# Optimization experiments

Measured on AMD Instinct MI355X. Metric: run time of the kernel, lower is better.

## Reference

```python
import jax, jax.numpy as jnp
import numpy as np

N = 100000
E = 1600000
IN_C = 256
OUT_C = 128


def setup_inputs() -> dict:
    key = jax.random.key(0)
    ks = jax.random.split(key, 8)
    x = jax.random.normal(ks[0], (N, IN_C), dtype=jnp.float32)
    edge_index = jax.random.randint(ks[1], (2, E), 0, N, dtype=jnp.int64)
    # GCNConv params (weight + bias)
    W = jax.random.normal(ks[2], (IN_C, OUT_C), dtype=jnp.float32) / np.sqrt(IN_C)
    b = jnp.zeros((OUT_C,), dtype=jnp.float32)
    # residual Linear params
    Wr = jax.random.normal(ks[3], (IN_C, OUT_C), dtype=jnp.float32) / np.sqrt(IN_C)
    br = jnp.zeros((OUT_C,), dtype=jnp.float32)
    # LayerNorm params
    gamma = jnp.ones((OUT_C,), dtype=jnp.float32)
    beta = jnp.zeros((OUT_C,), dtype=jnp.float32)
    return {"x": x, "edge_index": edge_index, "W": W, "b": b,
            "Wr": Wr, "br": br, "gamma": gamma, "beta": beta}


def _gcn_conv(x, src, dst, W, b):
    # PyG GCNConv: add self-loops, symmetric degree normalization,
    # transform first (out < in), then gather-scale-scatter.
    n = x.shape[0]
    loops = jnp.arange(n, dtype=src.dtype)
    src = jnp.concatenate([src, loops])
    dst = jnp.concatenate([dst, loops])
    ones = jnp.ones_like(dst, dtype=x.dtype)
    deg = jax.ops.segment_sum(ones, dst, num_segments=n)  # [N]
    dinv = jnp.where(deg > 0, jax.lax.rsqrt(deg), 0.0)
    norm = dinv[src] * dinv[dst]                           # [E+N]
    h = x @ W                                              # [N, out]
    msg = h[src] * norm[:, None]                           # [E+N, out]
    agg = jax.ops.segment_sum(msg, dst, num_segments=n)    # [N, out]
    return agg + b


def _layer_norm(x, gamma, beta, eps=1e-5):
    mu = jnp.mean(x, axis=-1, keepdims=True)
    var = jnp.mean(jnp.square(x - mu), axis=-1, keepdims=True)
    return (x - mu) * jax.lax.rsqrt(var + eps) * gamma + beta


def reference(x, edge_index, W, b, Wr, br, gamma, beta):
    src, dst = edge_index[0], edge_index[1]
    res = x @ Wr + br
    h = _gcn_conv(x, src, dst, W, b)
    out = _layer_norm(h + res, gamma, beta)
    return jax.nn.relu(out)
```

## Files before the change

### kernel.cpp

```cpp
#include <hip/hip_runtime.h>

typedef __attribute__((ext_vector_type(8))) short bf16x8;
typedef __attribute__((ext_vector_type(4))) float f32x4;
typedef __attribute__((ext_vector_type(8))) unsigned short ushort8;
typedef __attribute__((ext_vector_type(4))) unsigned short ushort4v;

__device__ __forceinline__ unsigned short f2bf(float f) {
  unsigned int u = __float_as_uint(f);
  u = u + 0x7FFFu + ((u >> 16) & 1u);
  return (unsigned short)(u >> 16);
}
__device__ __forceinline__ float bflo(unsigned int u) { return __uint_as_float(u << 16); }
__device__ __forceinline__ float bfhi(unsigned int u) { return __uint_as_float(u & 0xFFFF0000u); }

#define GLOAD_LDS16(g, l)                                                            \
  __builtin_amdgcn_global_load_lds((const __attribute__((address_space(1))) void*)(g), \
                                   (__attribute__((address_space(3))) void*)(l), 16, 0, 0)

__global__ void k_degrank(const int* __restrict__ dst, int* __restrict__ deg,
                          int* __restrict__ rank, int E) {
  int base = (blockIdx.x * blockDim.x + threadIdx.x) * 4;
  if (base + 3 < E) {
    int4 d = *(const int4*)(dst + base);
    int r0 = atomicAdd(&deg[d.x], 1);
    int r1 = atomicAdd(&deg[d.y], 1);
    int r2 = atomicAdd(&deg[d.z], 1);
    int r3 = atomicAdd(&deg[d.w], 1);
    *(int4*)(rank + base) = make_int4(r0, r1, r2, r3);
  } else {
    for (int e = base; e < E; ++e) rank[e] = atomicAdd(&deg[dst[e]], 1);
  }
}

__global__ void k_dinv(const int* __restrict__ deg, float* __restrict__ dinv, int N) {
  int i = blockIdx.x * blockDim.x + threadIdx.x;
  if (i < N) dinv[i] = rsqrtf((float)(deg[i] + 1));
}

__global__ void k_scanA(const int* __restrict__ deg, int* __restrict__ bsums, int N) {
  __shared__ int s[256];
  int t = threadIdx.x;
  int base = blockIdx.x * 1024 + t * 4;
  int ts = 0;
#pragma unroll
  for (int j = 0; j < 4; ++j) { int idx = base + j; ts += (idx < N) ? deg[idx] : 0; }
  s[t] = ts; __syncthreads();
  for (int off = 1; off < 256; off <<= 1) {
    int v = (t >= off) ? s[t - off] : 0;
    __syncthreads();
    s[t] += v;
    __syncthreads();
  }
  if (t == 255) bsums[blockIdx.x] = s[255];
}

__global__ void k_scanB(int* bsums, int nb) {
  __shared__ int s[128];
  int t = threadIdx.x;
  int v = (t < nb) ? bsums[t] : 0;
  s[t] = v; __syncthreads();
  for (int off = 1; off < 128; off <<= 1) {
    int a = (t >= off) ? s[t - off] : 0;
    __syncthreads();
    s[t] += a;
    __syncthreads();
  }
  if (t < nb) bsums[t] = s[t] - v;
}

__global__ void k_scanC(const int* __restrict__ deg, const int* __restrict__ bsums,
                        int* __restrict__ start, int N) {
  __shared__ int s[256];
  int t = threadIdx.x;
  int base = blockIdx.x * 1024 + t * 4;
  int v[4]; int ts = 0;
#pragma unroll
  for (int j = 0; j < 4; ++j) { int idx = base + j; v[j] = (idx < N) ? deg[idx] : 0; ts += v[j]; }
  s[t] = ts; __syncthreads();
  for (int off = 1; off < 256; off <<= 1) {
    int a = (t >= off) ? s[t - off] : 0;
    __syncthreads();
    s[t] += a;
    __syncthreads();
  }
  int run = bsums[blockIdx.x] + s[t] - ts;
#pragma unroll
  for (int j = 0; j < 4; ++j) { int idx = base + j; if (idx < N) start[idx] = run; run += v[j]; }
}

__global__ void k_fill(const int* __restrict__ src, const int* __restrict__ dst,
                       const int* __restrict__ start, const int* __restrict__ rank,
                       int* __restrict__ ssrc, int E) {
  int base = (blockIdx.x * blockDim.x + threadIdx.x) * 4;
  if (base + 3 < E) {
    int4 d = *(const int4*)(dst + base);
    int4 r = *(const int4*)(rank + base);
    int4 s = *(const int4*)(src + base);
    ssrc[start[d.x] + r.x] = s.x;
    ssrc[start[d.y] + r.y] = s.y;
    ssrc[start[d.z] + r.z] = s.z;
    ssrc[start[d.w] + r.w] = s.w;
  } else {
    for (int e = base; e < E; ++e) ssrc[start[dst[e]] + rank[e]] = src[e];
  }
}

__global__ void k_prepw(const float* __restrict__ W, const float* __restrict__ Wr,
                        unsigned short* __restrict__ Wb) {
  int t = blockIdx.x * 256 + threadIdx.x;
  if (t >= 2048) return;
  int col = t >> 3, g = t & 7;
  const float* Ws = (col < 128) ? (W + col) : (Wr + (col - 128));
#pragma unroll
  for (int kt = 0; kt < 4; ++kt) {
    ushort8 u;
#pragma unroll
    for (int j = 0; j < 8; ++j) u[j] = f2bf(Ws[(size_t)(kt * 64 + g * 8 + j) * 128]);
    *(ushort8*)&Wb[kt * 16384 + col * 64 + ((g ^ (col & 7)) * 8)] = u;
  }
}

__global__ __launch_bounds__(512) void k_gemm(
    const float* __restrict__ x, const unsigned short* __restrict__ Wb,
    const float* __restrict__ br, const float* __restrict__ dinv,
    unsigned short* __restrict__ hs, float* res, int N)
{
  __shared__ unsigned short xt[128][72];
  __shared__ unsigned short wt[256 * 64];
  int tid = threadIdx.x;
  int lane = tid & 63, w = tid >> 6;
  int lo = lane & 15, hi = lane >> 4;
  int brow = blockIdx.x * 128;

  f32x4 acc[16];
#pragma unroll
  for (int c = 0; c < 16; ++c) acc[c] = (f32x4){0.f, 0.f, 0.f, 0.f};

  for (int kt = 0; kt < 4; ++kt) {
    int k0 = kt * 64;
    const unsigned short* gw = Wb + kt * 16384;
#pragma unroll
    for (int i = 0; i < 4; ++i) {
      int off = i * 4096 + tid * 8;
      GLOAD_LDS16(gw + off, &wt[off]);
    }
#pragma unroll
    for (int r = 0; r < 4; ++r) {
      int idx = tid + 512 * r;
      int row = idx >> 4, kq = idx & 15;
      int node = brow + row;
      float4 v = make_float4(0.f, 0.f, 0.f, 0.f);
      if (node < N) v = *(const float4*)(x + (size_t)node * 256 + k0 + kq * 4);
      ushort4v u;
      u[0] = f2bf(v.x); u[1] = f2bf(v.y); u[2] = f2bf(v.z); u[3] = f2bf(v.w);
      *(ushort4v*)(&xt[row][kq * 4]) = u;
    }
    __syncthreads();
#pragma unroll
    for (int kk = 0; kk < 2; ++kk) {
      bf16x8 a = *(const bf16x8*)(&xt[w * 16 + lo][kk * 32 + hi * 8]);
      int gsw = ((kk * 4 + hi) ^ (lo & 7)) * 8;
#pragma unroll
      for (int c = 0; c < 16; ++c) {
        bf16x8 b = *(const bf16x8*)(&wt[(c * 16 + lo) * 64 + gsw]);
        acc[c] = __builtin_amdgcn_mfma_f32_16x16x32_bf16(a, b, acc[c], 0, 0, 0);
      }
    }
    __syncthreads();
  }
#pragma unroll
  for (int c = 0; c < 16; ++c) {
    int colo = c * 16 + lo;
#pragma unroll
    for (int rg = 0; rg < 4; ++rg) {
      int row = brow + w * 16 + hi * 4 + rg;
      if (row < N) {
        float v = acc[c][rg];
        if (colo < 128) hs[(size_t)row * 128 + colo] = f2bf(v * dinv[row]);
        else            res[(size_t)row * 128 + (colo - 128)] = v + br[colo - 128];
      }
    }
  }
}

__global__ __launch_bounds__(256) void k_agg(
    const unsigned int* __restrict__ hsb, const float* resin,
    const float* __restrict__ dinv, const int* __restrict__ start,
    const int* __restrict__ deg, const int* __restrict__ ssrc,
    const float* __restrict__ bias, const float* __restrict__ gamma,
    const float* __restrict__ beta, float* out, int N)
{
  int node = blockIdx.x * 4 + (threadIdx.x >> 6);
  int lane = threadIdx.x & 63;
  if (node >= N) return;
  unsigned int su = hsb[(size_t)node * 64 + lane];
  float ax = bflo(su), ay = bfhi(su);
  int s0 = start[node], cnt = deg[node];
  const int* sp = ssrc + s0;
  int e = 0;
  for (; e + 8 <= cnt; e += 8) {
    int i0 = sp[e + 0], i1 = sp[e + 1], i2 = sp[e + 2], i3 = sp[e + 3];
    int i4 = sp[e + 4], i5 = sp[e + 5], i6 = sp[e + 6], i7 = sp[e + 7];
    unsigned int u0 = hsb[(size_t)i0 * 64 + lane];
    unsigned int u1 = hsb[(size_t)i1 * 64 + lane];
    unsigned int u2 = hsb[(size_t)i2 * 64 + lane];
    unsigned int u3 = hsb[(size_t)i3 * 64 + lane];
    unsigned int u4 = hsb[(size_t)i4 * 64 + lane];
    unsigned int u5 = hsb[(size_t)i5 * 64 + lane];
    unsigned int u6 = hsb[(size_t)i6 * 64 + lane];
    unsigned int u7 = hsb[(size_t)i7 * 64 + lane];
    float x01 = bflo(u0) + bflo(u1), x23 = bflo(u2) + bflo(u3);
    float x45 = bflo(u4) + bflo(u5), x67 = bflo(u6) + bflo(u7);
    float y01 = bfhi(u0) + bfhi(u1), y23 = bfhi(u2) + bfhi(u3);
    float y45 = bfhi(u4) + bfhi(u5), y67 = bfhi(u6) + bfhi(u7);
    ax += (x01 + x23) + (x45 + x67);
    ay += (y01 + y23) + (y45 + y67);
  }
  for (; e + 4 <= cnt; e += 4) {
    int i0 = sp[e + 0], i1 = sp[e + 1], i2 = sp[e + 2], i3 = sp[e + 3];
    unsigned int u0 = hsb[(size_t)i0 * 64 + lane];
    unsigned int u1 = hsb[(size_t)i1 * 64 + lane];
    unsigned int u2 = hsb[(size_t)i2 * 64 + lane];
    unsigned int u3 = hsb[(size_t)i3 * 64 + lane];
    ax += (bflo(u0) + bflo(u1)) + (bflo(u2) + bflo(u3));
    ay += (bfhi(u0) + bfhi(u1)) + (bfhi(u2) + bfhi(u3));
  }
  for (; e < cnt; ++e) {
    int s = sp[e];
    unsigned int u = hsb[(size_t)s * 64 + lane];
    ax += bflo(u); ay += bfhi(u);
  }
  float di = dinv[node];
  float2 r  = ((const float2*)resin)[(size_t)node * 64 + lane];
  float2 bb = ((const float2*)bias)[lane];
  float vx = ax * di + bb.x + r.x;
  float vy = ay * di + bb.y + r.y;
  float sum = vx + vy;
#pragma unroll
  for (int off = 32; off >= 1; off >>= 1) sum += __shfl_xor(sum, off, 64);
  float mean = sum * (1.0f / 128.0f);
  float dx = vx - mean, dy = vy - mean;
  float sq = dx * dx + dy * dy;
#pragma unroll
  for (int off = 32; off >= 1; off >>= 1) sq += __shfl_xor(sq, off, 64);
  float rstd = rsqrtf(sq * (1.0f / 128.0f) + 1e-5f);
  float2 g  = ((const float2*)gamma)[lane];
  float2 be = ((const float2*)beta)[lane];
  float ox = fmaxf(dx * rstd * g.x + be.x, 0.0f);
  float oy = fmaxf(dy * rstd * g.y + be.y, 0.0f);
  ((float2*)out)[(size_t)node * 64 + lane] = make_float2(ox, oy);
}

extern "C" void kernel_launch(void* const* d_in, const int* in_sizes, int n_in,
                              void* d_out, int out_size, void* d_ws, size_t ws_size,
                              hipStream_t stream) {
  const float* x     = (const float*)d_in[0];
  const int*   eidx  = (const int*)d_in[1];
  const float* W     = (const float*)d_in[2];
  const float* b     = (const float*)d_in[3];
  const float* Wr    = (const float*)d_in[4];
  const float* br    = (const float*)d_in[5];
  const float* gamma = (const float*)d_in[6];
  const float* beta  = (const float*)d_in[7];
  float* out = (float*)d_out;

  int N = in_sizes[0] / 256;
  int E = in_sizes[1] / 2;
  const int* srcI = eidx;
  const int* dstI = eidx + E;

  char* w = (char*)d_ws;
  size_t off = 0;
  auto alloc = [&](size_t bytes) -> void* {
    void* p = w + off;
    off += (bytes + 255) & ~(size_t)255;
    return p;
  };
  unsigned short* hs   = (unsigned short*)alloc((size_t)N * 128 * 2);
  int*   deg    = (int*)alloc((size_t)N * 4);
  float* dinv   = (float*)alloc((size_t)N * 4);
  int*   start  = (int*)alloc((size_t)N * 4);
  int*   rank   = (int*)alloc((size_t)E * 4);
  int*   ssrc   = (int*)alloc((size_t)E * 4);
  unsigned short* Wb = (unsigned short*)alloc((size_t)4 * 16384 * 2);
  int nb = (N + 1023) / 1024;
  int*   bsums  = (int*)alloc(((size_t)nb + 32) * 4);

  hipMemsetAsync(deg, 0, (size_t)N * 4, stream);
  int egrid = (E / 4 + 255) / 256 + 1;
  k_degrank<<<egrid, 256, 0, stream>>>(dstI, deg, rank, E);
  k_dinv <<<(N + 255) / 256, 256, 0, stream>>>(deg, dinv, N);
  k_scanA<<<nb, 256, 0, stream>>>(deg, bsums, N);
  k_scanB<<<1, 128, 0, stream>>>(bsums, nb);
  k_scanC<<<nb, 256, 0, stream>>>(deg, bsums, start, N);
  k_fill <<<egrid, 256, 0, stream>>>(srcI, dstI, start, rank, ssrc, E);
  k_prepw<<<8, 256, 0, stream>>>(W, Wr, Wb);
  k_gemm <<<(N + 127) / 128, 512, 0, stream>>>(x, Wb, br, dinv, hs, out, N);
  k_agg  <<<(N + 3) / 4, 256, 0, stream>>>((const unsigned int*)hs, out, dinv, start, deg, ssrc,
                                           b, gamma, beta, out, N);
}
```

Measured before the change: 238.7 us.

## Fuse preprocessing kernels and overlap CSR fill with GEMM blocks

```diff
diff --git a/kernel.cpp b/kernel.cpp
--- a/kernel.cpp
+++ b/kernel.cpp
@@ -17,9 +17,24 @@
   __builtin_amdgcn_global_load_lds((const __attribute__((address_space(1))) void*)(g), \
                                    (__attribute__((address_space(3))) void*)(l), 16, 0, 0)
 
-__global__ void k_degrank(const int* __restrict__ dst, int* __restrict__ deg,
-                          int* __restrict__ rank, int E) {
-  int base = (blockIdx.x * blockDim.x + threadIdx.x) * 4;
+__global__ void k_prep_degrank(const float* __restrict__ W, const float* __restrict__ Wr,
+                               unsigned short* __restrict__ Wb,
+                               const int* __restrict__ dst, int* __restrict__ deg,
+                               int* __restrict__ rank, int E) {
+  if (blockIdx.x < 8) {
+    int t = blockIdx.x * 256 + threadIdx.x;
+    int col = t >> 3, g = t & 7;
+    const float* Ws = (col < 128) ? (W + col) : (Wr + (col - 128));
+#pragma unroll
+    for (int kt = 0; kt < 4; ++kt) {
+      ushort8 u;
+#pragma unroll
+      for (int j = 0; j < 8; ++j) u[j] = f2bf(Ws[(size_t)(kt * 64 + g * 8 + j) * 128]);
+      *(ushort8*)&Wb[kt * 16384 + col * 64 + ((g ^ (col & 7)) * 8)] = u;
+    }
+    return;
+  }
+  int base = ((blockIdx.x - 8) * 256 + threadIdx.x) * 4;
   if (base + 3 < E) {
     int4 d = *(const int4*)(dst + base);
     int r0 = atomicAdd(&deg[d.x], 1);
@@ -32,11 +47,6 @@
   }
 }
 
-__global__ void k_dinv(const int* __restrict__ deg, float* __restrict__ dinv, int N) {
-  int i = blockIdx.x * blockDim.x + threadIdx.x;
-  if (i < N) dinv[i] = rsqrtf((float)(deg[i] + 1));
-}
-
 __global__ void k_scanA(const int* __restrict__ deg, int* __restrict__ bsums, int N) {
   __shared__ int s[256];
   int t = threadIdx.x;
@@ -68,8 +78,8 @@
   if (t < nb) bsums[t] = s[t] - v;
 }
 
-__global__ void k_scanC(const int* __restrict__ deg, const int* __restrict__ bsums,
-                        int* __restrict__ start, int N) {
+__global__ void k_scanC_dinv(const int* __restrict__ deg, const int* __restrict__ bsums,
+                             int* __restrict__ start, float* __restrict__ dinv, int N) {
   __shared__ int s[256];
   int t = threadIdx.x;
   int base = blockIdx.x * 1024 + t * 4;
@@ -85,52 +95,47 @@
   }
   int run = bsums[blockIdx.x] + s[t] - ts;
 #pragma unroll
-  for (int j = 0; j < 4; ++j) { int idx = base + j; if (idx < N) start[idx] = run; run += v[j]; }
-}
-
-__global__ void k_fill(const int* __restrict__ src, const int* __restrict__ dst,
-                       const int* __restrict__ start, const int* __restrict__ rank,
-                       int* __restrict__ ssrc, int E) {
-  int base = (blockIdx.x * blockDim.x + threadIdx.x) * 4;
-  if (base + 3 < E) {
-    int4 d = *(const int4*)(dst + base);
-    int4 r = *(const int4*)(rank + base);
-    int4 s = *(const int4*)(src + base);
-    ssrc[start[d.x] + r.x] = s.x;
-    ssrc[start[d.y] + r.y] = s.y;
-    ssrc[start[d.z] + r.z] = s.z;
-    ssrc[start[d.w] + r.w] = s.w;
-  } else {
-    for (int e = base; e < E; ++e) ssrc[start[dst[e]] + rank[e]] = src[e];
-  }
-}
-
-__global__ void k_prepw(const float* __restrict__ W, const float* __restrict__ Wr,
-                        unsigned short* __restrict__ Wb) {
-  int t = blockIdx.x * 256 + threadIdx.x;
-  if (t >= 2048) return;
-  int col = t >> 3, g = t & 7;
-  const float* Ws = (col < 128) ? (W + col) : (Wr + (col - 128));
-#pragma unroll
-  for (int kt = 0; kt < 4; ++kt) {
-    ushort8 u;
-#pragma unroll
-    for (int j = 0; j < 8; ++j) u[j] = f2bf(Ws[(size_t)(kt * 64 + g * 8 + j) * 128]);
-    *(ushort8*)&Wb[kt * 16384 + col * 64 + ((g ^ (col & 7)) * 8)] = u;
-  }
-}
-
-__global__ __launch_bounds__(512) void k_gemm(
+  for (int j = 0; j < 4; ++j) {
+    int idx = base + j;
+    if (idx < N) {
+      start[idx] = run;
+      dinv[idx] = rsqrtf((float)(v[j] + 1));
+    }
+    run += v[j];
+  }
+}
+
+__global__ __launch_bounds__(512) void k_gemm_fill(
     const float* __restrict__ x, const unsigned short* __restrict__ Wb,
     const float* __restrict__ br, const float* __restrict__ dinv,
-    unsigned short* __restrict__ hs, float* res, int N)
+    unsigned short* __restrict__ hs, float* res, int N,
+    const int* __restrict__ src, const int* __restrict__ dst,
+    const int* __restrict__ start, const int* __restrict__ rank,
+    int* __restrict__ ssrc, int E)
 {
   __shared__ unsigned short xt[128][72];
   __shared__ unsigned short wt[256 * 64];
   int tid = threadIdx.x;
+
+  if (blockIdx.x & 1) {
+    int base = ((blockIdx.x >> 1) * 512 + tid) * 4;
+    if (base + 3 < E) {
+      int4 d = *(const int4*)(dst + base);
+      int4 r = *(const int4*)(rank + base);
+      int4 s = *(const int4*)(src + base);
+      ssrc[start[d.x] + r.x] = s.x;
+      ssrc[start[d.y] + r.y] = s.y;
+      ssrc[start[d.z] + r.z] = s.z;
+      ssrc[start[d.w] + r.w] = s.w;
+    } else {
+      for (int e = base; e < E; ++e) ssrc[start[dst[e]] + rank[e]] = src[e];
+    }
+    return;
+  }
+
   int lane = tid & 63, w = tid >> 6;
   int lo = lane & 15, hi = lane >> 4;
-  int brow = blockIdx.x * 128;
+  int brow = (blockIdx.x >> 1) * 128;
 
   f32x4 acc[16];
 #pragma unroll
@@ -287,15 +292,14 @@
   int*   bsums  = (int*)alloc(((size_t)nb + 32) * 4);
 
   hipMemsetAsync(deg, 0, (size_t)N * 4, stream);
-  int egrid = (E / 4 + 255) / 256 + 1;
-  k_degrank<<<egrid, 256, 0, stream>>>(dstI, deg, rank, E);
-  k_dinv <<<(N + 255) / 256, 256, 0, stream>>>(deg, dinv, N);
+  int dgrid = (E / 4 + 255) / 256;
+  k_prep_degrank<<<8 + dgrid, 256, 0, stream>>>(W, Wr, Wb, dstI, deg, rank, E);
   k_scanA<<<nb, 256, 0, stream>>>(deg, bsums, N);
   k_scanB<<<1, 128, 0, stream>>>(bsums, nb);
-  k_scanC<<<nb, 256, 0, stream>>>(deg, bsums, start, N);
-  k_fill <<<egrid, 256, 0, stream>>>(srcI, dstI, start, rank, ssrc, E);
-  k_prepw<<<8, 256, 0, stream>>>(W, Wr, Wb);
-  k_gemm <<<(N + 127) / 128, 512, 0, stream>>>(x, Wb, br, dinv, hs, out, N);
+  k_scanC_dinv<<<nb, 256, 0, stream>>>(deg, bsums, start, dinv, N);
+  int ggrid = (N + 127) / 128;
+  k_gemm_fill<<<2 * ggrid, 512, 0, stream>>>(x, Wb, br, dinv, hs, out, N,
+                                             srcI, dstI, start, rank, ssrc, E);
   k_agg  <<<(N + 3) / 4, 256, 0, stream>>>((const unsigned int*)hs, out, dinv, start, deg, ssrc,
                                            b, gamma, beta, out, N);
 }
```

Result: slower. 247.4 us (+3.6%).
